# Optimization experiments

Hardware: AMD Instinct MI355X
Metric: run time of the kernel (lower is better)

The kernel has to match this reference:

```python
import jax, jax.numpy as jnp
import numpy as np

N_NODES = 100000
N_EDGES = 3200000
IN_CH = 512
HIDDEN = 64
LOC_OUT = 16
OUT_CH = 40


def setup_inputs() -> dict:
    key = jax.random.key(0)
    ks = jax.random.split(key, 10)
    return {
        "batch_x": jax.random.normal(ks[0], (N_NODES, IN_CH), dtype=jnp.float32),
        "edge_index": jax.random.randint(ks[1], (2, N_EDGES), 0, N_NODES, dtype=jnp.int64),
        "glob_emb": jax.random.normal(ks[2], (N_NODES, LOC_OUT), dtype=jnp.float32),
        "W1": jax.random.normal(ks[3], (IN_CH, HIDDEN), dtype=jnp.float32) * (1.0 / np.sqrt(IN_CH)),
        "b1": jnp.zeros((HIDDEN,), dtype=jnp.float32),
        "W2": jax.random.normal(ks[4], (HIDDEN, LOC_OUT), dtype=jnp.float32) * (1.0 / np.sqrt(HIDDEN)),
        "b2": jnp.zeros((LOC_OUT,), dtype=jnp.float32),
        "att_w1": jax.random.normal(ks[5], (LOC_OUT, 16), dtype=jnp.float32) * 0.25,
        "att_b1": jnp.zeros((16,), dtype=jnp.float32),
        "att_w2": jax.random.normal(ks[6], (16, 1), dtype=jnp.float32) * 0.25,
        "lin1_w": jax.random.normal(ks[7], (LOC_OUT, OUT_CH), dtype=jnp.float32) * 0.25,
        "lin1_b": jnp.zeros((OUT_CH,), dtype=jnp.float32),
    }


def _gcn_conv(x, W, b, row, col, n):
    # GCNConv: out = D^-1/2 (A + I) D^-1/2 (X W) + b   (PyG default: self-loops, sym norm)
    h = x @ W
    loops = jnp.arange(n, dtype=row.dtype)
    row2 = jnp.concatenate([row, loops])  # sources (x_j)
    col2 = jnp.concatenate([col, loops])  # targets (aggregation index)
    deg = jax.ops.segment_sum(jnp.ones_like(col2, dtype=h.dtype), col2, num_segments=n)
    dinv = jax.lax.rsqrt(jnp.maximum(deg, 1.0))  # deg >= 1 thanks to self-loops
    norm = dinv[row2] * dinv[col2]               # [E+N]
    agg = jax.ops.segment_sum(h[row2] * norm[:, None], col2, num_segments=n)
    return agg + b


def reference(batch_x, edge_index, glob_emb, W1, b1, W2, b2, att_w1, att_b1, att_w2, lin1_w, lin1_b):
    n = batch_x.shape[0]
    row, col = edge_index[0], edge_index[1]
    x = _gcn_conv(batch_x, W1, b1, row, col, n)
    x = jax.nn.relu(x)  # dropout p=0.0 -> identity
    x = _gcn_conv(x, W2, b2, row, col, n)  # last layer: no relu/dropout
    z = jnp.stack([x, glob_emb], axis=1)  # [N, 2, 16]
    w = jnp.tanh(z @ att_w1 + att_b1) @ att_w2  # [N, 2, 1]
    beta = jax.nn.softmax(w, axis=1)
    emb = jnp.sum(beta * z, axis=1)  # [N, 16]
    return emb @ lin1_w + lin1_b  # [N, 40]
```

## Files before the change

### kernel.cpp

```cpp
#include <hip/hip_runtime.h>

#define N_IN 512
#define HID 64
#define NBLK 256

typedef __attribute__((ext_vector_type(4))) float f32x4;
typedef __attribute__((ext_vector_type(8))) short bf16x8;

__device__ inline float bf2f(unsigned short s) {
    union { unsigned int u; float f; } v; v.u = ((unsigned int)s) << 16; return v.f;
}
__device__ inline unsigned short f2bf(float f) {
    union { float f; unsigned int u; } v; v.f = f;
    unsigned int u = v.u;
    return (unsigned short)((u + 0x7FFFu + ((u >> 16) & 1u)) >> 16);
}

__global__ __launch_bounds__(1024) void k_histA_wt(const int* __restrict__ EI, int* __restrict__ hist,
                                                   const float* __restrict__ W1, unsigned short* __restrict__ Wt,
                                                   int E, int N, int K) {
    int tid = threadIdx.x;
    if (blockIdx.x >= NBLK) {
        int i = (blockIdx.x - NBLK) * 1024 + tid;
        if (i < N_IN * HID) {
            int k = i >> 6, n = i & 63;
            Wt[n * 512 + k] = f2bf(W1[i]);
        }
        return;
    }
    __shared__ int hs[512];
    __shared__ int sflag;
    if (tid == 0) sflag = (EI[1] == 0 && EI[3] == 0 && EI[5] == 0 && EI[7] == 0) ? 1 : 0;
    if (tid < 512) hs[tid] = 0;
    __syncthreads();
    bool f = sflag != 0;
    int chunk = (E + NBLK - 1) / NBLK;
    int s = blockIdx.x * chunk, e = min(E, s + chunk);
    for (int i = s + tid; i < e; i += 1024) {
        int c = f ? ((const int2*)EI)[E + i].x : EI[E + i];
        if ((unsigned)c < (unsigned)N) atomicAdd(&hs[c >> 8], 1);
    }
    __syncthreads();
    for (int k = tid; k < K; k += 1024) hist[k * NBLK + blockIdx.x] = hs[k];
}

__global__ __launch_bounds__(256) void k_scan_a2(int* __restrict__ data, int* __restrict__ bsum, int n) {
    __shared__ int sd[256];
    int i = blockIdx.x * 256 + threadIdx.x;
    int v = (i < n) ? data[i] : 0;
    sd[threadIdx.x] = v;
    __syncthreads();
    for (int off = 1; off < 256; off <<= 1) {
        int t = 0;
        if (threadIdx.x >= (unsigned)off) t = sd[threadIdx.x - off];
        __syncthreads();
        sd[threadIdx.x] += t;
        __syncthreads();
    }
    if (i < n) data[i] = sd[threadIdx.x] - v;
    if (threadIdx.x == 255) bsum[blockIdx.x] = sd[255];
}

__global__ __launch_bounds__(512) void k_scan_b(const int* __restrict__ bsum, int* __restrict__ bexc, int nb,
                                                unsigned short* __restrict__ h1, unsigned short* __restrict__ h2,
                                                int N) {
    __shared__ int sd[512];
    int t = threadIdx.x;
    if (t < 32) ((unsigned int*)(h1 + (size_t)N * 64))[t] = 0;
    if (t >= 32 && t < 40) ((unsigned int*)(h2 + (size_t)N * 16))[t - 32] = 0;
    int v = (t < nb) ? bsum[t] : 0;
    sd[t] = v;
    __syncthreads();
    for (int off = 1; off < 512; off <<= 1) {
        int u = 0;
        if (t >= off) u = sd[t - off];
        __syncthreads();
        sd[t] += u;
        __syncthreads();
    }
    if (t < nb) bexc[t] = sd[t] - v;
    if (t == 511) bexc[nb] = sd[511];
}

__global__ __launch_bounds__(1024) void k_partB(const int* __restrict__ EI, const int* __restrict__ hist,
                                                const int* __restrict__ bexc, int* __restrict__ edges2,
                                                int E, int N, int K) {
    __shared__ int cur[512];
    __shared__ int sflag;
    int tid = threadIdx.x, b = blockIdx.x;
    if (tid == 0) sflag = (EI[1] == 0 && EI[3] == 0 && EI[5] == 0 && EI[7] == 0) ? 1 : 0;
    if (tid < 512) cur[tid] = (tid < K) ? (bexc[tid] + hist[tid * NBLK + b]) : 0;
    __syncthreads();
    bool f = sflag != 0;
    int chunk = (E + NBLK - 1) / NBLK;
    int s = b * chunk, e = min(E, s + chunk);
    for (int i = s + tid; i < e; i += 1024) {
        int r, c;
        if (f) { const int2* E2 = (const int2*)EI; r = E2[i].x; c = E2[E + i].x; }
        else   { r = EI[i]; c = EI[E + i]; }
        if ((unsigned)r >= (unsigned)N || (unsigned)c >= (unsigned)N) continue;
        int pos = atomicAdd(&cur[c >> 8], 1);
        edges2[pos] = r | ((c & 255) << 20);
    }
}

__global__ __launch_bounds__(256) void k_gemm1(const float* __restrict__ X, const unsigned short* __restrict__ Wt,
                                               unsigned short* __restrict__ H, int N) {
    int tid = threadIdx.x;
    int w = tid >> 6, lane = tid & 63;
    int m_l = lane & 15, q = lane >> 4;
    int m0 = blockIdx.x * 128 + w * 32;
    int rA0 = m0 + m_l, rA1 = m0 + 16 + m_l;
    int rc0 = rA0 < N ? rA0 : N - 1;
    int rc1 = rA1 < N ? rA1 : N - 1;
    const float* baseA0 = X + (size_t)rc0 * 512 + q * 8;
    const float* baseA1 = X + (size_t)rc1 * 512 + q * 8;
    const unsigned short* baseB = Wt + (size_t)m_l * 512 + q * 8;

    f32x4 acc[2][4] = {};
#pragma unroll 4
    for (int c = 0; c < 16; ++c) {
        int ko = c * 32;
        float4 x0a = *(const float4*)(baseA0 + ko);
        float4 x0b = *(const float4*)(baseA0 + ko + 4);
        float4 x1a = *(const float4*)(baseA1 + ko);
        float4 x1b = *(const float4*)(baseA1 + ko + 4);
        bf16x8 a0, a1;
        a0[0] = (short)f2bf(x0a.x); a0[1] = (short)f2bf(x0a.y); a0[2] = (short)f2bf(x0a.z); a0[3] = (short)f2bf(x0a.w);
        a0[4] = (short)f2bf(x0b.x); a0[5] = (short)f2bf(x0b.y); a0[6] = (short)f2bf(x0b.z); a0[7] = (short)f2bf(x0b.w);
        a1[0] = (short)f2bf(x1a.x); a1[1] = (short)f2bf(x1a.y); a1[2] = (short)f2bf(x1a.z); a1[3] = (short)f2bf(x1a.w);
        a1[4] = (short)f2bf(x1b.x); a1[5] = (short)f2bf(x1b.y); a1[6] = (short)f2bf(x1b.z); a1[7] = (short)f2bf(x1b.w);
#pragma unroll
        for (int t = 0; t < 4; ++t) {
            bf16x8 bb = *(const bf16x8*)(baseB + (size_t)t * 16 * 512 + ko);
            acc[0][t] = __builtin_amdgcn_mfma_f32_16x16x32_bf16(a0, bb, acc[0][t], 0, 0, 0);
            acc[1][t] = __builtin_amdgcn_mfma_f32_16x16x32_bf16(a1, bb, acc[1][t], 0, 0, 0);
        }
    }
#pragma unroll
    for (int h = 0; h < 2; ++h) {
#pragma unroll
        for (int rg = 0; rg < 4; ++rg) {
            int row = m0 + h * 16 + q * 4 + rg;
            if (row < N) {
#pragma unroll
                for (int t = 0; t < 4; ++t)
                    H[(size_t)row * 64 + t * 16 + m_l] = f2bf(acc[h][t][rg]);
            }
        }
    }
}

__global__ __launch_bounds__(256) void k_bucket(const int* __restrict__ bexc, const int* __restrict__ edges2,
                                                int* __restrict__ edges, int* __restrict__ start,
                                                int* __restrict__ endv, float* __restrict__ dinv,
                                                unsigned short* __restrict__ H, int N, int K) {
    __shared__ int hist[256], sd[256], cur[256];
    __shared__ float dvs[256];
    int b = blockIdx.x, tid = threadIdx.x;
    int cbase = bexc[b];
    int cend  = bexc[b + 1];
    int base  = ((cbase + 3) & ~3) + 1024 * b;
    hist[tid] = 0;
    __syncthreads();
    for (int i = cbase + tid; i < cend; i += 256)
        atomicAdd(&hist[(edges2[i] >> 20) & 255], 1);
    __syncthreads();
    int v = hist[tid];
    int v4 = (v + 3) & ~3;
    sd[tid] = v4;
    __syncthreads();
    for (int off = 1; off < 256; off <<= 1) {
        int t = 0;
        if (tid >= off) t = sd[tid - off];
        __syncthreads();
        sd[tid] += t;
        __syncthreads();
    }
    int excl = sd[tid] - v4;
    cur[tid] = excl;
    int node = b * 256 + tid;
    float dvv = rsqrtf((float)(v + 1));
    dvs[tid] = dvv;
    if (node < N) {
        start[node] = base + excl;
        endv[node]  = base + excl + v;
        dinv[node]  = dvv;
    }
    __syncthreads();
    for (int i = cbase + tid; i < cend; i += 256) {
        int pv = edges2[i];
        int pos = atomicAdd(&cur[(pv >> 20) & 255], 1);
        edges[base + pos] = pv & 0xFFFFF;
    }
    for (int rr = tid >> 4; rr < 256; rr += 16) {
        int n2 = b * 256 + rr;
        if (n2 < N) {
            float dv2 = dvs[rr];
            uint2* pp = (uint2*)(H + (size_t)n2 * 64 + (size_t)(tid & 15) * 4);
            uint2 vv = *pp;
            float f0 = bf2f((unsigned short)(vv.x & 0xffffu)) * dv2;
            float f1 = bf2f((unsigned short)(vv.x >> 16)) * dv2;
            float f2 = bf2f((unsigned short)(vv.y & 0xffffu)) * dv2;
            float f3 = bf2f((unsigned short)(vv.y >> 16)) * dv2;
            vv.x = (unsigned int)f2bf(f0) | ((unsigned int)f2bf(f1) << 16);
            vv.y = (unsigned int)f2bf(f2) | ((unsigned int)f2bf(f3) << 16);
            *pp = vv;
        }
    }
}

__global__ __launch_bounds__(256) void k_agg1g2(const unsigned short* __restrict__ H, const int* __restrict__ edges,
                                                const int* __restrict__ start, const int* __restrict__ endv,
                                                const float* __restrict__ dinv,
                                                const float* __restrict__ b1, const float* __restrict__ W2,
                                                unsigned short* __restrict__ H2, int N) {
    __shared__ float w2s[64 * 17];
    int tid = threadIdx.x;
    for (int i = tid; i < 1024; i += 256) { int k = i >> 4, c = i & 15; w2s[k * 17 + c] = W2[i]; }
    __syncthreads();
    int wid = blockIdx.x * 4 + (tid >> 6);
    int lane = tid & 63;
    if (wid >= N) return;
    int g = lane >> 4;
    int c4 = lane & 15;
    const size_t coff = (size_t)c4 * 4;
    float a0 = 0.f, a1 = 0.f, a2 = 0.f, a3 = 0.f;
    int s = start[wid], e = endv[wid];
    int4 s0, s1;
    if (s < e) {
        s0 = *(const int4*)(edges + s + g * 4);
        s1 = *(const int4*)(edges + s + 16 + g * 4);
    }
    for (int i = s; i < e; i += 32) {
        int jb0 = i + g * 4, jb1 = i + 16 + g * 4;
        int i0 = (jb0 + 0 < e) ? s0.x : N;
        int i1 = (jb0 + 1 < e) ? s0.y : N;
        int i2 = (jb0 + 2 < e) ? s0.z : N;
        int i3 = (jb0 + 3 < e) ? s0.w : N;
        int i4 = (jb1 + 0 < e) ? s1.x : N;
        int i5 = (jb1 + 1 < e) ? s1.y : N;
        int i6 = (jb1 + 2 < e) ? s1.z : N;
        int i7 = (jb1 + 3 < e) ? s1.w : N;
        uint2 v0 = *(const uint2*)(H + (size_t)i0 * 64 + coff);
        uint2 v1 = *(const uint2*)(H + (size_t)i1 * 64 + coff);
        uint2 v2 = *(const uint2*)(H + (size_t)i2 * 64 + coff);
        uint2 v3 = *(const uint2*)(H + (size_t)i3 * 64 + coff);
        uint2 v4 = *(const uint2*)(H + (size_t)i4 * 64 + coff);
        uint2 v5 = *(const uint2*)(H + (size_t)i5 * 64 + coff);
        uint2 v6 = *(const uint2*)(H + (size_t)i6 * 64 + coff);
        uint2 v7 = *(const uint2*)(H + (size_t)i7 * 64 + coff);
        int ni = i + 32;
        if (ni < e) {
            s0 = *(const int4*)(edges + ni + g * 4);
            s1 = *(const int4*)(edges + ni + 16 + g * 4);
        }
        a0 += __uint_as_float(v0.x << 16) + __uint_as_float(v1.x << 16)
            + __uint_as_float(v2.x << 16) + __uint_as_float(v3.x << 16)
            + __uint_as_float(v4.x << 16) + __uint_as_float(v5.x << 16)
            + __uint_as_float(v6.x << 16) + __uint_as_float(v7.x << 16);
        a1 += __uint_as_float(v0.x & 0xffff0000u) + __uint_as_float(v1.x & 0xffff0000u)
            + __uint_as_float(v2.x & 0xffff0000u) + __uint_as_float(v3.x & 0xffff0000u)
            + __uint_as_float(v4.x & 0xffff0000u) + __uint_as_float(v5.x & 0xffff0000u)
            + __uint_as_float(v6.x & 0xffff0000u) + __uint_as_float(v7.x & 0xffff0000u);
        a2 += __uint_as_float(v0.y << 16) + __uint_as_float(v1.y << 16)
            + __uint_as_float(v2.y << 16) + __uint_as_float(v3.y << 16)
            + __uint_as_float(v4.y << 16) + __uint_as_float(v5.y << 16)
            + __uint_as_float(v6.y << 16) + __uint_as_float(v7.y << 16);
        a3 += __uint_as_float(v0.y & 0xffff0000u) + __uint_as_float(v1.y & 0xffff0000u)
            + __uint_as_float(v2.y & 0xffff0000u) + __uint_as_float(v3.y & 0xffff0000u)
            + __uint_as_float(v4.y & 0xffff0000u) + __uint_as_float(v5.y & 0xffff0000u)
            + __uint_as_float(v6.y & 0xffff0000u) + __uint_as_float(v7.y & 0xffff0000u);
    }
    a0 += __shfl_xor(a0, 16, 64); a0 += __shfl_xor(a0, 32, 64);
    a1 += __shfl_xor(a1, 16, 64); a1 += __shfl_xor(a1, 32, 64);
    a2 += __shfl_xor(a2, 16, 64); a2 += __shfl_xor(a2, 32, 64);
    a3 += __shfl_xor(a3, 16, 64); a3 += __shfl_xor(a3, 32, 64);
    float dv = dinv[wid];
    uint2 sv = *(const uint2*)(H + (size_t)wid * 64 + coff);
    a0 += __uint_as_float(sv.x << 16);
    a1 += __uint_as_float(sv.x & 0xffff0000u);
    a2 += __uint_as_float(sv.y << 16);
    a3 += __uint_as_float(sv.y & 0xffff0000u);
    float4 bv = *(const float4*)(b1 + c4 * 4);
    float r0 = fmaxf(a0 * dv + bv.x, 0.f);
    float r1 = fmaxf(a1 * dv + bv.y, 0.f);
    float r2 = fmaxf(a2 * dv + bv.z, 0.f);
    float r3 = fmaxf(a3 * dv + bv.w, 0.f);
    float p = 0.f;
#pragma unroll
    for (int j = 0; j < 4; ++j) {
        int src = 4 * g + j;
        float x0 = __shfl(r0, src, 64);
        float x1 = __shfl(r1, src, 64);
        float x2 = __shfl(r2, src, 64);
        float x3 = __shfl(r3, src, 64);
        int kb = 16 * g + 4 * j;
        p += x0 * w2s[(kb + 0) * 17 + c4];
        p += x1 * w2s[(kb + 1) * 17 + c4];
        p += x2 * w2s[(kb + 2) * 17 + c4];
        p += x3 * w2s[(kb + 3) * 17 + c4];
    }
    p += __shfl_xor(p, 16, 64);
    p += __shfl_xor(p, 32, 64);
    if (g == 0) H2[(size_t)wid * 16 + c4] = f2bf(p * dv);
}

__global__ __launch_bounds__(256) void k_agg2(const unsigned short* __restrict__ H2, const int* __restrict__ edges,
                                              const int* __restrict__ start, const int* __restrict__ endv,
                                              const float* __restrict__ dinv,
                                              const float* __restrict__ b2, float* __restrict__ X2, int N) {
    int wid = blockIdx.x * 4 + (threadIdx.x >> 6);
    int lane = threadIdx.x & 63;
    if (wid >= N) return;
    int g = lane >> 3;
    int c2 = lane & 7;
    const size_t coff = (size_t)c2 * 2;
    float a0 = 0.f, a1 = 0.f;
    int s = start[wid], e = endv[wid];
    int4 s0, s1;
    if (s < e) {
        s0 = *(const int4*)(edges + s + g * 4);
        s1 = *(const int4*)(edges + s + 32 + g * 4);
    }
    for (int i = s; i < e; i += 64) {
        int jb0 = i + g * 4, jb1 = i + 32 + g * 4;
        int i0 = (jb0 + 0 < e) ? s0.x : N;
        int i1 = (jb0 + 1 < e) ? s0.y : N;
        int i2 = (jb0 + 2 < e) ? s0.z : N;
        int i3 = (jb0 + 3 < e) ? s0.w : N;
        int i4 = (jb1 + 0 < e) ? s1.x : N;
        int i5 = (jb1 + 1 < e) ? s1.y : N;
        int i6 = (jb1 + 2 < e) ? s1.z : N;
        int i7 = (jb1 + 3 < e) ? s1.w : N;
        unsigned int v0 = *(const unsigned int*)(H2 + (size_t)i0 * 16 + coff);
        unsigned int v1 = *(const unsigned int*)(H2 + (size_t)i1 * 16 + coff);
        unsigned int v2 = *(const unsigned int*)(H2 + (size_t)i2 * 16 + coff);
        unsigned int v3 = *(const unsigned int*)(H2 + (size_t)i3 * 16 + coff);
        unsigned int v4 = *(const unsigned int*)(H2 + (size_t)i4 * 16 + coff);
        unsigned int v5 = *(const unsigned int*)(H2 + (size_t)i5 * 16 + coff);
        unsigned int v6 = *(const unsigned int*)(H2 + (size_t)i6 * 16 + coff);
        unsigned int v7 = *(const unsigned int*)(H2 + (size_t)i7 * 16 + coff);
        int ni = i + 64;
        if (ni < e) {
            s0 = *(const int4*)(edges + ni + g * 4);
            s1 = *(const int4*)(edges + ni + 32 + g * 4);
        }
        a0 += __uint_as_float(v0 << 16) + __uint_as_float(v1 << 16)
            + __uint_as_float(v2 << 16) + __uint_as_float(v3 << 16)
            + __uint_as_float(v4 << 16) + __uint_as_float(v5 << 16)
            + __uint_as_float(v6 << 16) + __uint_as_float(v7 << 16);
        a1 += __uint_as_float(v0 & 0xffff0000u) + __uint_as_float(v1 & 0xffff0000u)
            + __uint_as_float(v2 & 0xffff0000u) + __uint_as_float(v3 & 0xffff0000u)
            + __uint_as_float(v4 & 0xffff0000u) + __uint_as_float(v5 & 0xffff0000u)
            + __uint_as_float(v6 & 0xffff0000u) + __uint_as_float(v7 & 0xffff0000u);
    }
    a0 += __shfl_xor(a0, 8, 64); a0 += __shfl_xor(a0, 16, 64); a0 += __shfl_xor(a0, 32, 64);
    a1 += __shfl_xor(a1, 8, 64); a1 += __shfl_xor(a1, 16, 64); a1 += __shfl_xor(a1, 32, 64);
    if (g == 0) {
        float dv = dinv[wid];
        unsigned int sv = *(const unsigned int*)(H2 + (size_t)wid * 16 + coff);
        a0 += __uint_as_float(sv << 16);
        a1 += __uint_as_float(sv & 0xffff0000u);
        float2 bv = *(const float2*)(b2 + c2 * 2);
        float2 o; o.x = a0 * dv + bv.x; o.y = a1 * dv + bv.y;
        *(float2*)(X2 + (size_t)wid * 16 + coff) = o;
    }
}

__global__ __launch_bounds__(256) void k_head(const float* __restrict__ X2, const float* __restrict__ G,
                                              const float* __restrict__ AW1, const float* __restrict__ AB1,
                                              const float* __restrict__ AW2, const float* __restrict__ LW,
                                              const float* __restrict__ LB, float* __restrict__ OUT, int N) {
    __shared__ float s_aw1[256], s_ab1[16], s_aw2[16], s_lw[640], s_lb[40];
    int tid = threadIdx.x;
    s_aw1[tid] = AW1[tid];
    if (tid < 16) { s_ab1[tid] = AB1[tid]; s_aw2[tid] = AW2[tid]; }
    for (int i = tid; i < 640; i += 256) s_lw[i] = LW[i];
    if (tid < 40) s_lb[tid] = LB[tid];
    __syncthreads();
    int node = blockIdx.x * 256 + tid;
    if (node >= N) return;
    float x[16], g[16];
    const float4* xp = (const float4*)(X2 + (size_t)node * 16);
    const float4* gp = (const float4*)(G + (size_t)node * 16);
#pragma unroll
    for (int q = 0; q < 4; ++q) {
        float4 v = xp[q]; x[q*4] = v.x; x[q*4+1] = v.y; x[q*4+2] = v.z; x[q*4+3] = v.w;
        float4 u = gp[q]; g[q*4] = u.x; g[q*4+1] = u.y; g[q*4+2] = u.z; g[q*4+3] = u.w;
    }
    float wx = 0.f, wg = 0.f;
#pragma unroll
    for (int j = 0; j < 16; ++j) {
        float tx = s_ab1[j], tg = s_ab1[j];
#pragma unroll
        for (int c = 0; c < 16; ++c) { tx += x[c] * s_aw1[c*16 + j]; tg += g[c] * s_aw1[c*16 + j]; }
        wx += tanhf(tx) * s_aw2[j];
        wg += tanhf(tg) * s_aw2[j];
    }
    float m = fmaxf(wx, wg);
    float ex = expf(wx - m), eg = expf(wg - m);
    float inv = 1.f / (ex + eg);
    float bx = ex * inv, bg = eg * inv;
    float emb[16];
#pragma unroll
    for (int c = 0; c < 16; ++c) emb[c] = bx * x[c] + bg * g[c];
    float* op = OUT + (size_t)node * 40;
    for (int o = 0; o < 40; ++o) {
        float a = s_lb[o];
#pragma unroll
        for (int c = 0; c < 16; ++c) a += emb[c] * s_lw[c*40 + o];
        op[o] = a;
    }
}

extern "C" void kernel_launch(void* const* d_in, const int* in_sizes, int n_in,
                              void* d_out, int out_size, void* d_ws, size_t ws_size,
                              hipStream_t stream) {
    const float* X   = (const float*)d_in[0];
    const int*   EI  = (const int*)d_in[1];
    const float* G   = (const float*)d_in[2];
    const float* W1  = (const float*)d_in[3];
    const float* B1  = (const float*)d_in[4];
    const float* W2  = (const float*)d_in[5];
    const float* B2  = (const float*)d_in[6];
    const float* AW1 = (const float*)d_in[7];
    const float* AB1 = (const float*)d_in[8];
    const float* AW2 = (const float*)d_in[9];
    const float* LW  = (const float*)d_in[10];
    const float* LB  = (const float*)d_in[11];
    float* OUT = (float*)d_out;

    const int N = in_sizes[0] / N_IN;
    const int E = in_sizes[1] / 2;
    const int NB = (N + 255) / 256;
    const int K  = NB;
    const int NH = K * NBLK;
    const int SB = (NH + 255) / 256;
    const int WB = (N_IN * HID + 1023) / 1024;
    const int GB = (N + 127) / 128;

    char* w = (char*)d_ws;
    size_t off = 0;
    auto take = [&](size_t bytes) -> void* {
        void* p = (void*)(w + off);
        off = (off + bytes + 255) & ~(size_t)255;
        return p;
    };
    int*   hist   = (int*)take((size_t)NH * 4);
    int*   bsum   = (int*)take((size_t)SB * 4);
    int*   bexc   = (int*)take((size_t)(SB + 1) * 4);
    int*   startp = (int*)take((size_t)N * 4);
    int*   endp   = (int*)take((size_t)N * 4);
    float* dinvp  = (float*)take((size_t)N * 4);
    int*   edges2 = (int*)take((size_t)E * 4);
    int*   edges  = (int*)take((size_t)(E + 1024 * (size_t)K + 256) * 4);
    unsigned short* wt = (unsigned short*)take((size_t)N_IN * HID * 2);
    unsigned short* h1 = (unsigned short*)take((size_t)(N + 1) * 64 * 2);
    unsigned short* h2 = (unsigned short*)take((size_t)(N + 1) * 16 * 2);
    float* x2 = (float*)take((size_t)N * 16 * 4);
    (void)ws_size; (void)n_in; (void)out_size;

    k_histA_wt<<<NBLK + WB, 1024, 0, stream>>>(EI, hist, W1, wt, E, N, K);
    k_scan_a2 <<<SB, 256, 0, stream>>>(hist, bsum, NH);
    k_scan_b  <<<1, 512, 0, stream>>>(bsum, bexc, SB, h1, h2, N);
    k_partB   <<<NBLK, 1024, 0, stream>>>(EI, hist, bexc, edges2, E, N, K);
    k_gemm1   <<<GB, 256, 0, stream>>>(X, wt, h1, N);
    k_bucket  <<<K, 256, 0, stream>>>(bexc, edges2, edges, startp, endp, dinvp, h1, N, K);
    k_agg1g2  <<<(N + 3) / 4, 256, 0, stream>>>(h1, edges, startp, endp, dinvp, B1, W2, h2, N);
    k_agg2    <<<(N + 3) / 4, 256, 0, stream>>>(h2, edges, startp, endp, dinvp, B2, x2, N);
    k_head    <<<NB, 256, 0, stream>>>(x2, G, AW1, AB1, AW2, LW, LB, OUT, N);
}
```

Baseline: 531.4 us.

## Widen gather loads in aggregation kernels and coalesce head output via LDS

The layer-1 aggregation now has each lane load 16-byte chunks (8 bf16 channels) with 8 lanes per row, so 8 edge groups are processed per iteration. The W2 projection is reorganized through shuffles to match the new layout. The layer-2 aggregation switches from 4-byte to 8-byte loads and covers 128 edges per iteration, at the cost of a longer shuffle reduction. The head kernel stages its 40-wide output rows in padded shared memory and writes them out coalesced instead of doing strided per-thread stores, which adds about 41 KB of LDS per block and may lower occupancy.

```diff
diff --git a/kernel.cpp b/kernel.cpp
--- a/kernel.cpp
+++ b/kernel.cpp
@@ -210,6 +210,16 @@
     }
 }
 
+#define ACC8(v) do { \
+    a[0] += __uint_as_float((v).x << 16); \
+    a[1] += __uint_as_float((v).x & 0xffff0000u); \
+    a[2] += __uint_as_float((v).y << 16); \
+    a[3] += __uint_as_float((v).y & 0xffff0000u); \
+    a[4] += __uint_as_float((v).z << 16); \
+    a[5] += __uint_as_float((v).z & 0xffff0000u); \
+    a[6] += __uint_as_float((v).w << 16); \
+    a[7] += __uint_as_float((v).w & 0xffff0000u); } while (0)
+
 __global__ __launch_bounds__(256) void k_agg1g2(const unsigned short* __restrict__ H, const int* __restrict__ edges,
                                                 const int* __restrict__ start, const int* __restrict__ endv,
                                                 const float* __restrict__ dinv,
@@ -222,38 +232,113 @@
     int wid = blockIdx.x * 4 + (tid >> 6);
     int lane = tid & 63;
     if (wid >= N) return;
-    int g = lane >> 4;
-    int c4 = lane & 15;
+    int g8 = (lane >> 3) * 8;
+    int c8 = lane & 7;
+    const size_t coff = (size_t)c8 * 8;
+    float a[8] = {0.f, 0.f, 0.f, 0.f, 0.f, 0.f, 0.f, 0.f};
+    int s = start[wid], e = endv[wid];
+    int4 s0, s1;
+    if (s < e) {
+        s0 = *(const int4*)(edges + s + g8);
+        s1 = *(const int4*)(edges + s + g8 + 4);
+    }
+    for (int i = s; i < e; i += 64) {
+        int jb = i + g8;
+        int i0 = (jb + 0 < e) ? s0.x : N;
+        int i1 = (jb + 1 < e) ? s0.y : N;
+        int i2 = (jb + 2 < e) ? s0.z : N;
+        int i3 = (jb + 3 < e) ? s0.w : N;
+        int i4 = (jb + 4 < e) ? s1.x : N;
+        int i5 = (jb + 5 < e) ? s1.y : N;
+        int i6 = (jb + 6 < e) ? s1.z : N;
+        int i7 = (jb + 7 < e) ? s1.w : N;
+        uint4 v0 = *(const uint4*)(H + (size_t)i0 * 64 + coff);
+        uint4 v1 = *(const uint4*)(H + (size_t)i1 * 64 + coff);
+        uint4 v2 = *(const uint4*)(H + (size_t)i2 * 64 + coff);
+        uint4 v3 = *(const uint4*)(H + (size_t)i3 * 64 + coff);
+        uint4 v4 = *(const uint4*)(H + (size_t)i4 * 64 + coff);
+        uint4 v5 = *(const uint4*)(H + (size_t)i5 * 64 + coff);
+        uint4 v6 = *(const uint4*)(H + (size_t)i6 * 64 + coff);
+        uint4 v7 = *(const uint4*)(H + (size_t)i7 * 64 + coff);
+        int ni = i + 64;
+        if (ni < e) {
+            s0 = *(const int4*)(edges + ni + g8);
+            s1 = *(const int4*)(edges + ni + g8 + 4);
+        }
+        ACC8(v0); ACC8(v1); ACC8(v2); ACC8(v3);
+        ACC8(v4); ACC8(v5); ACC8(v6); ACC8(v7);
+    }
+#pragma unroll
+    for (int c = 0; c < 8; ++c) {
+        a[c] += __shfl_xor(a[c], 8, 64);
+        a[c] += __shfl_xor(a[c], 16, 64);
+        a[c] += __shfl_xor(a[c], 32, 64);
+    }
+    float dv = dinv[wid];
+    uint4 sv = *(const uint4*)(H + (size_t)wid * 64 + coff);
+    ACC8(sv);
+    float4 bva = *(const float4*)(b1 + c8 * 8);
+    float4 bvb = *(const float4*)(b1 + c8 * 8 + 4);
+    float r[8];
+    r[0] = fmaxf(a[0] * dv + bva.x, 0.f);
+    r[1] = fmaxf(a[1] * dv + bva.y, 0.f);
+    r[2] = fmaxf(a[2] * dv + bva.z, 0.f);
+    r[3] = fmaxf(a[3] * dv + bva.w, 0.f);
+    r[4] = fmaxf(a[4] * dv + bvb.x, 0.f);
+    r[5] = fmaxf(a[5] * dv + bvb.y, 0.f);
+    r[6] = fmaxf(a[6] * dv + bvb.z, 0.f);
+    r[7] = fmaxf(a[7] * dv + bvb.w, 0.f);
+    int qt = lane >> 4, co = lane & 15;
+    float p = 0.f;
+#pragma unroll
+    for (int j = 0; j < 16; ++j) {
+        float xk = __shfl(r[j & 7], qt * 2 + (j >> 3), 64);
+        p += xk * w2s[(qt * 16 + j) * 17 + co];
+    }
+    p += __shfl_xor(p, 16, 64);
+    p += __shfl_xor(p, 32, 64);
+    if (lane < 16) H2[(size_t)wid * 16 + co] = f2bf(p * dv);
+}
+
+__global__ __launch_bounds__(256) void k_agg2(const unsigned short* __restrict__ H2, const int* __restrict__ edges,
+                                              const int* __restrict__ start, const int* __restrict__ endv,
+                                              const float* __restrict__ dinv,
+                                              const float* __restrict__ b2, float* __restrict__ X2, int N) {
+    int wid = blockIdx.x * 4 + (threadIdx.x >> 6);
+    int lane = threadIdx.x & 63;
+    if (wid >= N) return;
+    int g8 = (lane >> 2) * 8;
+    int c4 = lane & 3;
     const size_t coff = (size_t)c4 * 4;
     float a0 = 0.f, a1 = 0.f, a2 = 0.f, a3 = 0.f;
     int s = start[wid], e = endv[wid];
     int4 s0, s1;
     if (s < e) {
-        s0 = *(const int4*)(edges + s + g * 4);
-        s1 = *(const int4*)(edges + s + 16 + g * 4);
-    }
-    for (int i = s; i < e; i += 32) {
-        int jb0 = i + g * 4, jb1 = i + 16 + g * 4;
-        int i0 = (jb0 + 0 < e) ? s0.x : N;
-        int i1 = (jb0 + 1 < e) ? s0.y : N;
-        int i2 = (jb0 + 2 < e) ? s0.z : N;
-        int i3 = (jb0 + 3 < e) ? s0.w : N;
-        int i4 = (jb1 + 0 < e) ? s1.x : N;
-        int i5 = (jb1 + 1 < e) ? s1.y : N;
-        int i6 = (jb1 + 2 < e) ? s1.z : N;
-        int i7 = (jb1 + 3 < e) ? s1.w : N;
-        uint2 v0 = *(const uint2*)(H + (size_t)i0 * 64 + coff);
-        uint2 v1 = *(const uint2*)(H + (size_t)i1 * 64 + coff);
-        uint2 v2 = *(const uint2*)(H + (size_t)i2 * 64 + coff);
-        uint2 v3 = *(const uint2*)(H + (size_t)i3 * 64 + coff);
-        uint2 v4 = *(const uint2*)(H + (size_t)i4 * 64 + coff);
-        uint2 v5 = *(const uint2*)(H + (size_t)i5 * 64 + coff);
-        uint2 v6 = *(const uint2*)(H + (size_t)i6 * 64 + coff);
-        uint2 v7 = *(const uint2*)(H + (size_t)i7 * 64 + coff);
-        int ni = i + 32;
+        s0 = *(const int4*)(edges + s + g8);
+        s1 = *(const int4*)(edges + s + g8 + 4);
+    }
+    for (int i = s; i < e; i += 128) {
+        int jb = i + g8;
+        int i0 = (jb + 0 < e) ? s0.x : N;
+        int i1 = (jb + 1 < e) ? s0.y : N;
+        int i2 = (jb + 2 < e) ? s0.z : N;
+        int i3 = (jb + 3 < e) ? s0.w : N;
+        int i4 = (jb + 4 < e) ? s1.x : N;
+        int i5 = (jb + 5 < e) ? s1.y : N;
+        int i6 = (jb + 6 < e) ? s1.z : N;
+        int i7 = (jb + 7 < e) ? s1.w : N;
+        uint2 v0 = *(const uint2*)(H2 + (size_t)i0 * 16 + coff);
+        uint2 v1 = *(const uint2*)(H2 + (size_t)i1 * 16 + coff);
+        uint2 v2 = *(const uint2*)(H2 + (size_t)i2 * 16 + coff);
+        uint2 v3 = *(const uint2*)(H2 + (size_t)i3 * 16 + coff);
+        uint2 v4 = *(const uint2*)(H2 + (size_t)i4 * 16 + coff);
+        uint2 v5 = *(const uint2*)(H2 + (size_t)i5 * 16 + coff);
+        uint2 v6 = *(const uint2*)(H2 + (size_t)i6 * 16 + coff);
+        uint2 v7 = *(const uint2*)(H2 + (size_t)i7 * 16 + coff);
+        int ni = i + 128;
         if (ni < e) {
-            s0 = *(const int4*)(edges + ni + g * 4);
-            s1 = *(const int4*)(edges + ni + 16 + g * 4);
+            s0 = *(const int4*)(edges + ni + g8);
+            s1 = *(const int4*)(edges + ni + g8 + 4);
         }
         a0 += __uint_as_float(v0.x << 16) + __uint_as_float(v1.x << 16)
             + __uint_as_float(v2.x << 16) + __uint_as_float(v3.x << 16)
@@ -272,99 +357,22 @@
             + __uint_as_float(v4.y & 0xffff0000u) + __uint_as_float(v5.y & 0xffff0000u)
             + __uint_as_float(v6.y & 0xffff0000u) + __uint_as_float(v7.y & 0xffff0000u);
     }
-    a0 += __shfl_xor(a0, 16, 64); a0 += __shfl_xor(a0, 32, 64);
-    a1 += __shfl_xor(a1, 16, 64); a1 += __shfl_xor(a1, 32, 64);
-    a2 += __shfl_xor(a2, 16, 64); a2 += __shfl_xor(a2, 32, 64);
-    a3 += __shfl_xor(a3, 16, 64); a3 += __shfl_xor(a3, 32, 64);
-    float dv = dinv[wid];
-    uint2 sv = *(const uint2*)(H + (size_t)wid * 64 + coff);
-    a0 += __uint_as_float(sv.x << 16);
-    a1 += __uint_as_float(sv.x & 0xffff0000u);
-    a2 += __uint_as_float(sv.y << 16);
-    a3 += __uint_as_float(sv.y & 0xffff0000u);
-    float4 bv = *(const float4*)(b1 + c4 * 4);
-    float r0 = fmaxf(a0 * dv + bv.x, 0.f);
-    float r1 = fmaxf(a1 * dv + bv.y, 0.f);
-    float r2 = fmaxf(a2 * dv + bv.z, 0.f);
-    float r3 = fmaxf(a3 * dv + bv.w, 0.f);
-    float p = 0.f;
-#pragma unroll
-    for (int j = 0; j < 4; ++j) {
-        int src = 4 * g + j;
-        float x0 = __shfl(r0, src, 64);
-        float x1 = __shfl(r1, src, 64);
-        float x2 = __shfl(r2, src, 64);
-        float x3 = __shfl(r3, src, 64);
-        int kb = 16 * g + 4 * j;
-        p += x0 * w2s[(kb + 0) * 17 + c4];
-        p += x1 * w2s[(kb + 1) * 17 + c4];
-        p += x2 * w2s[(kb + 2) * 17 + c4];
-        p += x3 * w2s[(kb + 3) * 17 + c4];
-    }
-    p += __shfl_xor(p, 16, 64);
-    p += __shfl_xor(p, 32, 64);
-    if (g == 0) H2[(size_t)wid * 16 + c4] = f2bf(p * dv);
-}
-
-__global__ __launch_bounds__(256) void k_agg2(const unsigned short* __restrict__ H2, const int* __restrict__ edges,
-                                              const int* __restrict__ start, const int* __restrict__ endv,
-                                              const float* __restrict__ dinv,
-                                              const float* __restrict__ b2, float* __restrict__ X2, int N) {
-    int wid = blockIdx.x * 4 + (threadIdx.x >> 6);
-    int lane = threadIdx.x & 63;
-    if (wid >= N) return;
-    int g = lane >> 3;
-    int c2 = lane & 7;
-    const size_t coff = (size_t)c2 * 2;
-    float a0 = 0.f, a1 = 0.f;
-    int s = start[wid], e = endv[wid];
-    int4 s0, s1;
-    if (s < e) {
-        s0 = *(const int4*)(edges + s + g * 4);
-        s1 = *(const int4*)(edges + s + 32 + g * 4);
-    }
-    for (int i = s; i < e; i += 64) {
-        int jb0 = i + g * 4, jb1 = i + 32 + g * 4;
-        int i0 = (jb0 + 0 < e) ? s0.x : N;
-        int i1 = (jb0 + 1 < e) ? s0.y : N;
-        int i2 = (jb0 + 2 < e) ? s0.z : N;
-        int i3 = (jb0 + 3 < e) ? s0.w : N;
-        int i4 = (jb1 + 0 < e) ? s1.x : N;
-        int i5 = (jb1 + 1 < e) ? s1.y : N;
-        int i6 = (jb1 + 2 < e) ? s1.z : N;
-        int i7 = (jb1 + 3 < e) ? s1.w : N;
-        unsigned int v0 = *(const unsigned int*)(H2 + (size_t)i0 * 16 + coff);
-        unsigned int v1 = *(const unsigned int*)(H2 + (size_t)i1 * 16 + coff);
-        unsigned int v2 = *(const unsigned int*)(H2 + (size_t)i2 * 16 + coff);
-        unsigned int v3 = *(const unsigned int*)(H2 + (size_t)i3 * 16 + coff);
-        unsigned int v4 = *(const unsigned int*)(H2 + (size_t)i4 * 16 + coff);
-        unsigned int v5 = *(const unsigned int*)(H2 + (size_t)i5 * 16 + coff);
-        unsigned int v6 = *(const unsigned int*)(H2 + (size_t)i6 * 16 + coff);
-        unsigned int v7 = *(const unsigned int*)(H2 + (size_t)i7 * 16 + coff);
-        int ni = i + 64;
-        if (ni < e) {
-            s0 = *(const int4*)(edges + ni + g * 4);
-            s1 = *(const int4*)(edges + ni + 32 + g * 4);
-        }
-        a0 += __uint_as_float(v0 << 16) + __uint_as_float(v1 << 16)
-            + __uint_as_float(v2 << 16) + __uint_as_float(v3 << 16)
-            + __uint_as_float(v4 << 16) + __uint_as_float(v5 << 16)
-            + __uint_as_float(v6 << 16) + __uint_as_float(v7 << 16);
-        a1 += __uint_as_float(v0 & 0xffff0000u) + __uint_as_float(v1 & 0xffff0000u)
-            + __uint_as_float(v2 & 0xffff0000u) + __uint_as_float(v3 & 0xffff0000u)
-            + __uint_as_float(v4 & 0xffff0000u) + __uint_as_float(v5 & 0xffff0000u)
-            + __uint_as_float(v6 & 0xffff0000u) + __uint_as_float(v7 & 0xffff0000u);
-    }
-    a0 += __shfl_xor(a0, 8, 64); a0 += __shfl_xor(a0, 16, 64); a0 += __shfl_xor(a0, 32, 64);
-    a1 += __shfl_xor(a1, 8, 64); a1 += __shfl_xor(a1, 16, 64); a1 += __shfl_xor(a1, 32, 64);
-    if (g == 0) {
+    a0 += __shfl_xor(a0, 4, 64); a0 += __shfl_xor(a0, 8, 64); a0 += __shfl_xor(a0, 16, 64); a0 += __shfl_xor(a0, 32, 64);
+    a1 += __shfl_xor(a1, 4, 64); a1 += __shfl_xor(a1, 8, 64); a1 += __shfl_xor(a1, 16, 64); a1 += __shfl_xor(a1, 32, 64);
+    a2 += __shfl_xor(a2, 4, 64); a2 += __shfl_xor(a2, 8, 64); a2 += __shfl_xor(a2, 16, 64); a2 += __shfl_xor(a2, 32, 64);
+    a3 += __shfl_xor(a3, 4, 64); a3 += __shfl_xor(a3, 8, 64); a3 += __shfl_xor(a3, 16, 64); a3 += __shfl_xor(a3, 32, 64);
+    if (lane < 4) {
         float dv = dinv[wid];
-        unsigned int sv = *(const unsigned int*)(H2 + (size_t)wid * 16 + coff);
-        a0 += __uint_as_float(sv << 16);
-        a1 += __uint_as_float(sv & 0xffff0000u);
-        float2 bv = *(const float2*)(b2 + c2 * 2);
-        float2 o; o.x = a0 * dv + bv.x; o.y = a1 * dv + bv.y;
-        *(float2*)(X2 + (size_t)wid * 16 + coff) = o;
+        uint2 sv = *(const uint2*)(H2 + (size_t)wid * 16 + coff);
+        a0 += __uint_as_float(sv.x << 16);
+        a1 += __uint_as_float(sv.x & 0xffff0000u);
+        a2 += __uint_as_float(sv.y << 16);
+        a3 += __uint_as_float(sv.y & 0xffff0000u);
+        float4 bv = *(const float4*)(b2 + c4 * 4);
+        float4 o;
+        o.x = a0 * dv + bv.x; o.y = a1 * dv + bv.y;
+        o.z = a2 * dv + bv.z; o.w = a3 * dv + bv.w;
+        *(float4*)(X2 + (size_t)wid * 16 + c4 * 4) = o;
     }
 }
 
@@ -373,44 +381,52 @@
                                               const float* __restrict__ AW2, const float* __restrict__ LW,
                                               const float* __restrict__ LB, float* __restrict__ OUT, int N) {
     __shared__ float s_aw1[256], s_ab1[16], s_aw2[16], s_lw[640], s_lb[40];
+    __shared__ float s_out[256 * 41];
     int tid = threadIdx.x;
     s_aw1[tid] = AW1[tid];
     if (tid < 16) { s_ab1[tid] = AB1[tid]; s_aw2[tid] = AW2[tid]; }
     for (int i = tid; i < 640; i += 256) s_lw[i] = LW[i];
     if (tid < 40) s_lb[tid] = LB[tid];
     __syncthreads();
-    int node = blockIdx.x * 256 + tid;
-    if (node >= N) return;
-    float x[16], g[16];
-    const float4* xp = (const float4*)(X2 + (size_t)node * 16);
-    const float4* gp = (const float4*)(G + (size_t)node * 16);
-#pragma unroll
-    for (int q = 0; q < 4; ++q) {
-        float4 v = xp[q]; x[q*4] = v.x; x[q*4+1] = v.y; x[q*4+2] = v.z; x[q*4+3] = v.w;
-        float4 u = gp[q]; g[q*4] = u.x; g[q*4+1] = u.y; g[q*4+2] = u.z; g[q*4+3] = u.w;
-    }
-    float wx = 0.f, wg = 0.f;
-#pragma unroll
-    for (int j = 0; j < 16; ++j) {
-        float tx = s_ab1[j], tg = s_ab1[j];
-#pragma unroll
-        for (int c = 0; c < 16; ++c) { tx += x[c] * s_aw1[c*16 + j]; tg += g[c] * s_aw1[c*16 + j]; }
-        wx += tanhf(tx) * s_aw2[j];
-        wg += tanhf(tg) * s_aw2[j];
-    }
-    float m = fmaxf(wx, wg);
-    float ex = expf(wx - m), eg = expf(wg - m);
-    float inv = 1.f / (ex + eg);
-    float bx = ex * inv, bg = eg * inv;
-    float emb[16];
-#pragma unroll
-    for (int c = 0; c < 16; ++c) emb[c] = bx * x[c] + bg * g[c];
-    float* op = OUT + (size_t)node * 40;
-    for (int o = 0; o < 40; ++o) {
-        float a = s_lb[o];
-#pragma unroll
-        for (int c = 0; c < 16; ++c) a += emb[c] * s_lw[c*40 + o];
-        op[o] = a;
+    int node0 = blockIdx.x * 256;
+    int node = node0 + tid;
+    if (node < N) {
+        float x[16], g[16];
+        const float4* xp = (const float4*)(X2 + (size_t)node * 16);
+        const float4* gp = (const float4*)(G + (size_t)node * 16);
+#pragma unroll
+        for (int q = 0; q < 4; ++q) {
+            float4 v = xp[q]; x[q*4] = v.x; x[q*4+1] = v.y; x[q*4+2] = v.z; x[q*4+3] = v.w;
+            float4 u = gp[q]; g[q*4] = u.x; g[q*4+1] = u.y; g[q*4+2] = u.z; g[q*4+3] = u.w;
+        }
+        float wx = 0.f, wg = 0.f;
+#pragma unroll
+        for (int j = 0; j < 16; ++j) {
+            float tx = s_ab1[j], tg = s_ab1[j];
+#pragma unroll
+            for (int c = 0; c < 16; ++c) { tx += x[c] * s_aw1[c*16 + j]; tg += g[c] * s_aw1[c*16 + j]; }
+            wx += tanhf(tx) * s_aw2[j];
+            wg += tanhf(tg) * s_aw2[j];
+        }
+        float m = fmaxf(wx, wg);
+        float ex = expf(wx - m), eg = expf(wg - m);
+        float inv = 1.f / (ex + eg);
+        float bx = ex * inv, bg = eg * inv;
+        float emb[16];
+#pragma unroll
+        for (int c = 0; c < 16; ++c) emb[c] = bx * x[c] + bg * g[c];
+        for (int o = 0; o < 40; ++o) {
+            float a = s_lb[o];
+#pragma unroll
+            for (int c = 0; c < 16; ++c) a += emb[c] * s_lw[c*40 + o];
+            s_out[tid * 41 + o] = a;
+        }
+    }
+    __syncthreads();
+    int lim = min(256, N - node0) * 40;
+    for (int i = tid; i < lim; i += 256) {
+        int r = i / 40, c = i - r * 40;
+        OUT[(size_t)node0 * 40 + i] = s_out[r * 41 + c];
     }
 }
 
```

New measurement: 555.7 us. +4.6%, slower.

## Fold dinv scaling into GEMM epilogue and fuse attention head into agg2

Applied to the files above, without the earlier changes.

Reorders launches so bucketing (which computes dinv) runs before the first GEMM, letting the GEMM epilogue apply the per-row dinv scale and removing the separate read-modify-write pass over H1 in k_bucket. The attention/softmax/linear head is fused into the second aggregation kernel, with one wavefront per node computing the attention scores in parallel lanes and writing 40 outputs directly. This drops the x2 intermediate buffer and one kernel launch. The cost is that the head kernel now loads its weights into shared memory per 4-node block and does more shuffles per node.

```diff
diff --git a/kernel.cpp b/kernel.cpp
--- a/kernel.cpp
+++ b/kernel.cpp
@@ -104,8 +104,50 @@
     }
 }
 
+__global__ __launch_bounds__(256) void k_bucket(const int* __restrict__ bexc, const int* __restrict__ edges2,
+                                                int* __restrict__ edges, int* __restrict__ start,
+                                                int* __restrict__ endv, float* __restrict__ dinv,
+                                                int N, int K) {
+    __shared__ int hist[256], sd[256], cur[256];
+    int b = blockIdx.x, tid = threadIdx.x;
+    int cbase = bexc[b];
+    int cend  = bexc[b + 1];
+    int base  = ((cbase + 3) & ~3) + 1024 * b;
+    hist[tid] = 0;
+    __syncthreads();
+    for (int i = cbase + tid; i < cend; i += 256)
+        atomicAdd(&hist[(edges2[i] >> 20) & 255], 1);
+    __syncthreads();
+    int v = hist[tid];
+    int v4 = (v + 3) & ~3;
+    sd[tid] = v4;
+    __syncthreads();
+    for (int off = 1; off < 256; off <<= 1) {
+        int t = 0;
+        if (tid >= off) t = sd[tid - off];
+        __syncthreads();
+        sd[tid] += t;
+        __syncthreads();
+    }
+    int excl = sd[tid] - v4;
+    cur[tid] = excl;
+    int node = b * 256 + tid;
+    if (node < N) {
+        start[node] = base + excl;
+        endv[node]  = base + excl + v;
+        dinv[node]  = rsqrtf((float)(v + 1));
+    }
+    __syncthreads();
+    for (int i = cbase + tid; i < cend; i += 256) {
+        int pv = edges2[i];
+        int pos = atomicAdd(&cur[(pv >> 20) & 255], 1);
+        edges[base + pos] = pv & 0xFFFFF;
+    }
+}
+
 __global__ __launch_bounds__(256) void k_gemm1(const float* __restrict__ X, const unsigned short* __restrict__ Wt,
-                                               unsigned short* __restrict__ H, int N) {
+                                               const float* __restrict__ dinv, unsigned short* __restrict__ H,
+                                               int N) {
     int tid = threadIdx.x;
     int w = tid >> 6, lane = tid & 63;
     int m_l = lane & 15, q = lane >> 4;
@@ -143,69 +185,11 @@
         for (int rg = 0; rg < 4; ++rg) {
             int row = m0 + h * 16 + q * 4 + rg;
             if (row < N) {
+                float dv = dinv[row];
 #pragma unroll
                 for (int t = 0; t < 4; ++t)
-                    H[(size_t)row * 64 + t * 16 + m_l] = f2bf(acc[h][t][rg]);
+                    H[(size_t)row * 64 + t * 16 + m_l] = f2bf(acc[h][t][rg] * dv);
             }
-        }
-    }
-}
-
-__global__ __launch_bounds__(256) void k_bucket(const int* __restrict__ bexc, const int* __restrict__ edges2,
-                                                int* __restrict__ edges, int* __restrict__ start,
-                                                int* __restrict__ endv, float* __restrict__ dinv,
-                                                unsigned short* __restrict__ H, int N, int K) {
-    __shared__ int hist[256], sd[256], cur[256];
-    __shared__ float dvs[256];
-    int b = blockIdx.x, tid = threadIdx.x;
-    int cbase = bexc[b];
-    int cend  = bexc[b + 1];
-    int base  = ((cbase + 3) & ~3) + 1024 * b;
-    hist[tid] = 0;
-    __syncthreads();
-    for (int i = cbase + tid; i < cend; i += 256)
-        atomicAdd(&hist[(edges2[i] >> 20) & 255], 1);
-    __syncthreads();
-    int v = hist[tid];
-    int v4 = (v + 3) & ~3;
-    sd[tid] = v4;
-    __syncthreads();
-    for (int off = 1; off < 256; off <<= 1) {
-        int t = 0;
-        if (tid >= off) t = sd[tid - off];
-        __syncthreads();
-        sd[tid] += t;
-        __syncthreads();
-    }
-    int excl = sd[tid] - v4;
-    cur[tid] = excl;
-    int node = b * 256 + tid;
-    float dvv = rsqrtf((float)(v + 1));
-    dvs[tid] = dvv;
-    if (node < N) {
-        start[node] = base + excl;
-        endv[node]  = base + excl + v;
-        dinv[node]  = dvv;
-    }
-    __syncthreads();
-    for (int i = cbase + tid; i < cend; i += 256) {
-        int pv = edges2[i];
-        int pos = atomicAdd(&cur[(pv >> 20) & 255], 1);
-        edges[base + pos] = pv & 0xFFFFF;
-    }
-    for (int rr = tid >> 4; rr < 256; rr += 16) {
-        int n2 = b * 256 + rr;
-        if (n2 < N) {
-            float dv2 = dvs[rr];
-            uint2* pp = (uint2*)(H + (size_t)n2 * 64 + (size_t)(tid & 15) * 4);
-            uint2 vv = *pp;
-            float f0 = bf2f((unsigned short)(vv.x & 0xffffu)) * dv2;
-            float f1 = bf2f((unsigned short)(vv.x >> 16)) * dv2;
-            float f2 = bf2f((unsigned short)(vv.y & 0xffffu)) * dv2;
-            float f3 = bf2f((unsigned short)(vv.y >> 16)) * dv2;
-            vv.x = (unsigned int)f2bf(f0) | ((unsigned int)f2bf(f1) << 16);
-            vv.y = (unsigned int)f2bf(f2) | ((unsigned int)f2bf(f3) << 16);
-            *pp = vv;
         }
     }
 }
@@ -306,12 +290,22 @@
     if (g == 0) H2[(size_t)wid * 16 + c4] = f2bf(p * dv);
 }
 
-__global__ __launch_bounds__(256) void k_agg2(const unsigned short* __restrict__ H2, const int* __restrict__ edges,
-                                              const int* __restrict__ start, const int* __restrict__ endv,
-                                              const float* __restrict__ dinv,
-                                              const float* __restrict__ b2, float* __restrict__ X2, int N) {
-    int wid = blockIdx.x * 4 + (threadIdx.x >> 6);
-    int lane = threadIdx.x & 63;
+__global__ __launch_bounds__(256) void k_agg2h(const unsigned short* __restrict__ H2, const int* __restrict__ edges,
+                                               const int* __restrict__ start, const int* __restrict__ endv,
+                                               const float* __restrict__ dinv, const float* __restrict__ b2,
+                                               const float* __restrict__ G,
+                                               const float* __restrict__ AW1, const float* __restrict__ AB1,
+                                               const float* __restrict__ AW2, const float* __restrict__ LW,
+                                               const float* __restrict__ LB, float* __restrict__ OUT, int N) {
+    __shared__ float s_aw1[256], s_ab1[16], s_aw2[16], s_lw[640], s_lb[40];
+    int tid = threadIdx.x;
+    s_aw1[tid] = AW1[tid];
+    if (tid < 16) { s_ab1[tid] = AB1[tid]; s_aw2[tid] = AW2[tid]; }
+    for (int i = tid; i < 640; i += 256) s_lw[i] = LW[i];
+    if (tid < 40) s_lb[tid] = LB[tid];
+    __syncthreads();
+    int wid = blockIdx.x * 4 + (tid >> 6);
+    int lane = tid & 63;
     if (wid >= N) return;
     int g = lane >> 3;
     int c2 = lane & 7;
@@ -357,60 +351,42 @@
     }
     a0 += __shfl_xor(a0, 8, 64); a0 += __shfl_xor(a0, 16, 64); a0 += __shfl_xor(a0, 32, 64);
     a1 += __shfl_xor(a1, 8, 64); a1 += __shfl_xor(a1, 16, 64); a1 += __shfl_xor(a1, 32, 64);
-    if (g == 0) {
-        float dv = dinv[wid];
-        unsigned int sv = *(const unsigned int*)(H2 + (size_t)wid * 16 + coff);
-        a0 += __uint_as_float(sv << 16);
-        a1 += __uint_as_float(sv & 0xffff0000u);
-        float2 bv = *(const float2*)(b2 + c2 * 2);
-        float2 o; o.x = a0 * dv + bv.x; o.y = a1 * dv + bv.y;
-        *(float2*)(X2 + (size_t)wid * 16 + coff) = o;
-    }
-}
-
-__global__ __launch_bounds__(256) void k_head(const float* __restrict__ X2, const float* __restrict__ G,
-                                              const float* __restrict__ AW1, const float* __restrict__ AB1,
-                                              const float* __restrict__ AW2, const float* __restrict__ LW,
-                                              const float* __restrict__ LB, float* __restrict__ OUT, int N) {
-    __shared__ float s_aw1[256], s_ab1[16], s_aw2[16], s_lw[640], s_lb[40];
-    int tid = threadIdx.x;
-    s_aw1[tid] = AW1[tid];
-    if (tid < 16) { s_ab1[tid] = AB1[tid]; s_aw2[tid] = AW2[tid]; }
-    for (int i = tid; i < 640; i += 256) s_lw[i] = LW[i];
-    if (tid < 40) s_lb[tid] = LB[tid];
-    __syncthreads();
-    int node = blockIdx.x * 256 + tid;
-    if (node >= N) return;
-    float x[16], g[16];
-    const float4* xp = (const float4*)(X2 + (size_t)node * 16);
-    const float4* gp = (const float4*)(G + (size_t)node * 16);
+    float dv = dinv[wid];
+    unsigned int sv = *(const unsigned int*)(H2 + (size_t)wid * 16 + coff);
+    a0 += __uint_as_float(sv << 16);
+    a1 += __uint_as_float(sv & 0xffff0000u);
+    float2 bv = *(const float2*)(b2 + c2 * 2);
+    a0 = a0 * dv + bv.x;
+    a1 = a1 * dv + bv.y;
+    float x[16];
+#pragma unroll
+    for (int c = 0; c < 16; ++c) x[c] = __shfl((c & 1) ? a1 : a0, c >> 1, 64);
+    float gl[16];
+    const float4* gp = (const float4*)(G + (size_t)wid * 16);
 #pragma unroll
     for (int q = 0; q < 4; ++q) {
-        float4 v = xp[q]; x[q*4] = v.x; x[q*4+1] = v.y; x[q*4+2] = v.z; x[q*4+3] = v.w;
-        float4 u = gp[q]; g[q*4] = u.x; g[q*4+1] = u.y; g[q*4+2] = u.z; g[q*4+3] = u.w;
-    }
-    float wx = 0.f, wg = 0.f;
-#pragma unroll
-    for (int j = 0; j < 16; ++j) {
-        float tx = s_ab1[j], tg = s_ab1[j];
-#pragma unroll
-        for (int c = 0; c < 16; ++c) { tx += x[c] * s_aw1[c*16 + j]; tg += g[c] * s_aw1[c*16 + j]; }
-        wx += tanhf(tx) * s_aw2[j];
-        wg += tanhf(tg) * s_aw2[j];
-    }
+        float4 u = gp[q];
+        gl[q * 4] = u.x; gl[q * 4 + 1] = u.y; gl[q * 4 + 2] = u.z; gl[q * 4 + 3] = u.w;
+    }
+    int j = lane & 15;
+    bool isg = (lane >> 4) & 1;
+    float t = s_ab1[j];
+#pragma unroll
+    for (int c = 0; c < 16; ++c) t += (isg ? gl[c] : x[c]) * s_aw1[c * 16 + j];
+    float u = tanhf(t) * s_aw2[j];
+    u += __shfl_xor(u, 1, 64); u += __shfl_xor(u, 2, 64);
+    u += __shfl_xor(u, 4, 64); u += __shfl_xor(u, 8, 64);
+    float wx = __shfl(u, 0, 64);
+    float wg = __shfl(u, 16, 64);
     float m = fmaxf(wx, wg);
     float ex = expf(wx - m), eg = expf(wg - m);
     float inv = 1.f / (ex + eg);
     float bx = ex * inv, bg = eg * inv;
-    float emb[16];
-#pragma unroll
-    for (int c = 0; c < 16; ++c) emb[c] = bx * x[c] + bg * g[c];
-    float* op = OUT + (size_t)node * 40;
-    for (int o = 0; o < 40; ++o) {
-        float a = s_lb[o];
-#pragma unroll
-        for (int c = 0; c < 16; ++c) a += emb[c] * s_lw[c*40 + o];
-        op[o] = a;
+    if (lane < 40) {
+        float acc = s_lb[lane];
+#pragma unroll
+        for (int c = 0; c < 16; ++c) acc += (bx * x[c] + bg * gl[c]) * s_lw[c * 40 + lane];
+        OUT[(size_t)wid * 40 + lane] = acc;
     }
 }
 
@@ -458,16 +434,15 @@
     unsigned short* wt = (unsigned short*)take((size_t)N_IN * HID * 2);
     unsigned short* h1 = (unsigned short*)take((size_t)(N + 1) * 64 * 2);
     unsigned short* h2 = (unsigned short*)take((size_t)(N + 1) * 16 * 2);
-    float* x2 = (float*)take((size_t)N * 16 * 4);
     (void)ws_size; (void)n_in; (void)out_size;
 
     k_histA_wt<<<NBLK + WB, 1024, 0, stream>>>(EI, hist, W1, wt, E, N, K);
     k_scan_a2 <<<SB, 256, 0, stream>>>(hist, bsum, NH);
     k_scan_b  <<<1, 512, 0, stream>>>(bsum, bexc, SB, h1, h2, N);
     k_partB   <<<NBLK, 1024, 0, stream>>>(EI, hist, bexc, edges2, E, N, K);
-    k_gemm1   <<<GB, 256, 0, stream>>>(X, wt, h1, N);
-    k_bucket  <<<K, 256, 0, stream>>>(bexc, edges2, edges, startp, endp, dinvp, h1, N, K);
+    k_bucket  <<<K, 256, 0, stream>>>(bexc, edges2, edges, startp, endp, dinvp, N, K);
+    k_gemm1   <<<GB, 256, 0, stream>>>(X, wt, dinvp, h1, N);
     k_agg1g2  <<<(N + 3) / 4, 256, 0, stream>>>(h1, edges, startp, endp, dinvp, B1, W2, h2, N);
-    k_agg2    <<<(N + 3) / 4, 256, 0, stream>>>(h2, edges, startp, endp, dinvp, B2, x2, N);
-    k_head    <<<NB, 256, 0, stream>>>(x2, G, AW1, AB1, AW2, LW, LB, OUT, N);
-}
+    k_agg2h   <<<(N + 3) / 4, 256, 0, stream>>>(h2, edges, startp, endp, dinvp, B2, G,
+                                                AW1, AB1, AW2, LW, LB, OUT, N);
+}
```

Result: slower. 547.9 us (+3.1%).
